# Kernel optimization log

Measured on AMD Instinct MI355X. Metric: run time of the kernel, lower is better.

The kernel has to match this reference:

```python
import jax, jax.numpy as jnp
import numpy as np

B, S, C = 8, 2048, 1024
DROPOUT_RATE = 0.1


def setup_inputs() -> dict:
    key = jax.random.key(0)
    k1, k2, k3 = jax.random.split(key, 3)
    x = jax.random.normal(k1, (B, S, C), dtype=jnp.float32)
    # Fixed orthogonal projection buffer, as in __init__: U from SVD of a random matrix
    rand_mat = jax.random.normal(k2, (C, C), dtype=jnp.float32)
    U, _, _ = jnp.linalg.svd(rand_mat)
    U = U.astype(jnp.float32)
    # Base random permutation of [0, C)
    perm = jax.random.permutation(k3, C).astype(jnp.int32)
    # Stand-in for random.randint(0, 1000), fixed for determinism
    randint = 123
    return {"x": x, "U": U, "perm": perm, "randint": randint}


def reference(x, U, perm, randint):
    # channel_dim == -1, so the transpose in the original forward is a no-op.
    rand_scale = (DROPOUT_RATE / (1.0 - DROPOUT_RATE)) ** 0.5
    n = x.shape[-1]
    b = x.size // n
    # _randperm_like: per-row permutation ans[b_, i] = perm[i] * (6*randint*b_ + 1) mod n.
    # Reduce the multiplier mod n first so int32 arithmetic never overflows
    # (math is identical since (a*b) % n == (a*(b%n)) % n).
    batch_rand = (jnp.arange(b, dtype=jnp.int32) * (randint * 6) + 1) % n  # [b]
    ans = (perm[None, :] * batch_rand[:, None]) % n                        # [b, n]
    ans = ans.reshape(x.shape)                                             # same shape as x

    x_g = jnp.take_along_axis(x, ans, axis=-1)   # gather per-row permuted channels
    y = jnp.matmul(x_g, U)                        # shared (C,C) projection
    # scatter_(-1, ans, y) places y[..., j] at position ans[..., j]; since ans is a
    # permutation per row, this equals gathering y with the inverse permutation.
    inv = jnp.argsort(ans, axis=-1)
    x_next = jnp.take_along_axis(y, inv, axis=-1)
    return x_next * rand_scale + x
```

## Files before the change

### kernel.cpp

```cpp
#include <hip/hip_runtime.h>
#include <hip/hip_bf16.h>

#define WS_UT    ((size_t)0)
#define WS_XG    ((size_t)2*1024*1024)

typedef __attribute__((ext_vector_type(8))) short short8;
typedef __attribute__((ext_vector_type(4))) float floatx4;

__device__ __forceinline__ void load_lds16(const void* g, void* l) {
  __builtin_amdgcn_global_load_lds(
      (const __attribute__((address_space(1))) void*)g,
      (__attribute__((address_space(3))) void*)l, 16, 0, 0);
}

__device__ __forceinline__ unsigned short f2bf(float f) {
  __hip_bfloat16 h = __float2bfloat16(f);
  return __builtin_bit_cast(unsigned short, h);
}
__device__ __forceinline__ float bf2f(unsigned short u) {
  return __uint_as_float(((unsigned)u) << 16);
}

__global__ void __launch_bounds__(256) prep_gather_k(const float* __restrict__ U,
                                                     const float* __restrict__ x,
                                                     const int* __restrict__ perm,
                                                     const int* __restrict__ prand,
                                                     unsigned short* __restrict__ ut,
                                                     unsigned short* __restrict__ xg) {
  __shared__ __align__(16) char smem[64 * 65 * 4];
  if (blockIdx.x < 256) {
    float (*tile)[65] = (float (*)[65])smem;
    const int tn = (blockIdx.x & 15) * 64;
    const int tk = (blockIdx.x >> 4) * 64;
    const int r = threadIdx.x >> 6;
    const int c = threadIdx.x & 63;
    for (int s = 0; s < 16; ++s)
      tile[s * 4 + r][c] = U[(size_t)(tk + s * 4 + r) * 1024 + tn + c];
    __syncthreads();
    for (int s = 0; s < 16; ++s)
      ut[(size_t)(tn + s * 4 + r) * 1024 + tk + c] = f2bf(tile[c][s * 4 + r]);
    return;
  }
  float (*xrow)[1024] = (float (*)[1024])smem;
  const int w = threadIdx.x >> 6, lane = threadIdx.x & 63;
  const int row = (blockIdx.x - 256) * 4 + w;
  const unsigned mult = ((unsigned)prand[0] * 6u) & 1023u;
  const unsigned br = (((unsigned)row & 1023u) * mult + 1u) & 1023u;
  const float* xr = x + (size_t)row * 1024;
  unsigned short* xo = xg + (size_t)row * 1024;
  for (int t = 0; t < 4; ++t) {
    floatx4 v = *(const floatx4*)(xr + t * 256 + lane * 4);
    *(floatx4*)(&xrow[w][t * 256 + lane * 4]) = v;
  }
  __syncthreads();
  for (int t = 0; t < 4; ++t) {
    int i0 = t * 256 + lane * 4;
    int4 p = *(const int4*)(perm + i0);
    ushort4 o;
    o.x = f2bf(xrow[w][((unsigned)p.x * br) & 1023u]);
    o.y = f2bf(xrow[w][((unsigned)p.y * br) & 1023u]);
    o.z = f2bf(xrow[w][((unsigned)p.z * br) & 1023u]);
    o.w = f2bf(xrow[w][((unsigned)p.w * br) & 1023u]);
    *(ushort4*)(xo + i0) = o;
  }
}

__global__ void __launch_bounds__(512, 2) gemm_scatter_k(
    const unsigned short* __restrict__ xg,
    const unsigned short* __restrict__ ut,
    const int* __restrict__ perm,
    const int* __restrict__ prand,
    float* __restrict__ out) {
  extern __shared__ __align__(16) char smem[];
  const int tid = threadIdx.x;
  const int w = tid >> 6, lane = tid & 63;
  const int m = lane & 15, q = lane >> 4;
  const int R0 = blockIdx.x * 64;
  const int wn = w * 128;

  const int swz0 = (q ^ (m & 7)) * 16;
  const int vA0 = m * 128 + swz0;
  const int vA1 = vA0 ^ 64;
  const int vB0 = 24576 + w * 16384 + m * 128 + swz0;
  const int vB1 = vB0 ^ 64;

  const unsigned short* asrc =
      xg + (size_t)(R0 + (tid >> 3)) * 1024 + (size_t)(((tid & 7) ^ ((tid >> 3) & 7)) * 8);
  const unsigned short* bsrc0 =
      ut + (size_t)(wn + (lane >> 3)) * 1024 + (size_t)(((lane & 7) ^ (lane >> 3)) * 8);
  char* bdst0 = smem + 24576 + w * 16384 + lane * 16;

  floatx4 acc[4][8];
#pragma unroll
  for (int i = 0; i < 4; ++i)
#pragma unroll
    for (int jj = 0; jj < 8; ++jj) acc[i][jj] = (floatx4)0.0f;

  load_lds16(asrc, smem + tid * 16);
#pragma unroll
  for (int t = 0; t < 16; ++t)
    load_lds16(bsrc0 + (size_t)t * 8192, bdst0 + t * 1024);
  load_lds16(asrc + 64, smem + 8192 + tid * 16);
  asm volatile("s_waitcnt vmcnt(1)" ::: "memory");
  __builtin_amdgcn_sched_barrier(0);
  __builtin_amdgcn_s_barrier();
  __builtin_amdgcn_sched_barrier(0);

#pragma unroll
  for (int kt = 0; kt < 16; ++kt) {
    const int ab = (kt % 3) * 8192;
    short8 a0[4];
#pragma unroll
    for (int i = 0; i < 4; ++i)
      a0[i] = *(const short8*)(smem + ab + i * 2048 + vA0);
    if (kt > 0) {
      asm volatile("s_waitcnt vmcnt(1)" ::: "memory");
      __builtin_amdgcn_sched_barrier(0);
    }
    __builtin_amdgcn_s_setprio(1);
#pragma unroll
    for (int jj = 0; jj < 8; ++jj) {
      short8 b = *(const short8*)(smem + jj * 2048 + vB0);
#pragma unroll
      for (int i = 0; i < 4; ++i)
        acc[i][jj] = __builtin_amdgcn_mfma_f32_16x16x32_bf16(b, a0[i], acc[i][jj], 0, 0, 0);
    }
    short8 a1[4];
#pragma unroll
    for (int i = 0; i < 4; ++i)
      a1[i] = *(const short8*)(smem + ab + i * 2048 + vA1);
#pragma unroll
    for (int jj = 0; jj < 8; ++jj) {
      short8 b = *(const short8*)(smem + jj * 2048 + vB1);
#pragma unroll
      for (int i = 0; i < 4; ++i)
        acc[i][jj] = __builtin_amdgcn_mfma_f32_16x16x32_bf16(b, a1[i], acc[i][jj], 0, 0, 0);
    }
    __builtin_amdgcn_s_setprio(0);
    if (kt < 15) {
      asm volatile("s_waitcnt lgkmcnt(0)" ::: "memory");
      __builtin_amdgcn_sched_barrier(0);
      const int k1 = (kt + 1) * 64;
#pragma unroll
      for (int t = 0; t < 16; ++t)
        load_lds16(bsrc0 + (size_t)t * 8192 + k1, bdst0 + t * 1024);
      if (kt < 14)
        load_lds16(asrc + (size_t)(kt + 2) * 64, smem + ((kt + 2) % 3) * 8192 + tid * 16);
      if (kt < 14) asm volatile("s_waitcnt vmcnt(17)" ::: "memory");
      else         asm volatile("s_waitcnt vmcnt(16)" ::: "memory");
      __builtin_amdgcn_sched_barrier(0);
      __builtin_amdgcn_s_barrier();
      __builtin_amdgcn_sched_barrier(0);
    }
  }
  __syncthreads();

  const unsigned mult = ((unsigned)prand[0] * 6u) & 1023u;
  const float rs = 0.33333334f;
  float* sbuf = (float*)(smem + 24576);
#pragma unroll
  for (int p = 0; p < 8; ++p) {
    const int i = p >> 1;
    if ((m >> 3) == (p & 1)) {
      const int r = i * 16 + m;
      const unsigned br = (((unsigned)(R0 + r) & 1023u) * mult + 1u) & 1023u;
      const unsigned short* xr = xg + (size_t)(R0 + r) * 1024;
#pragma unroll
      for (int jj = 0; jj < 8; ++jj) {
        const int j0 = wn + jj * 16 + q * 4;
        const int4 p4 = *(const int4*)(perm + j0);
        const ushort4 x4 = *(const ushort4*)(xr + j0);
        sbuf[((r & 7) << 10) + (((unsigned)p4.x * br) & 1023u)] = rs * acc[i][jj][0] + bf2f(x4.x);
        sbuf[((r & 7) << 10) + (((unsigned)p4.y * br) & 1023u)] = rs * acc[i][jj][1] + bf2f(x4.y);
        sbuf[((r & 7) << 10) + (((unsigned)p4.z * br) & 1023u)] = rs * acc[i][jj][2] + bf2f(x4.z);
        sbuf[((r & 7) << 10) + (((unsigned)p4.w * br) & 1023u)] = rs * acc[i][jj][3] + bf2f(x4.w);
      }
    }
    __syncthreads();
    float* orow = out + (size_t)(R0 + p * 8) * 1024;
#pragma unroll
    for (int v = 0; v < 4; ++v) {
      const int f = v * 512 + tid;
      *(floatx4*)(orow + (size_t)f * 4) = *(const floatx4*)(sbuf + (size_t)f * 4);
    }
    if (p < 7) __syncthreads();
  }
}

extern "C" void kernel_launch(void* const* d_in, const int* in_sizes, int n_in,
                              void* d_out, int out_size, void* d_ws, size_t ws_size,
                              hipStream_t stream) {
  const float* x = (const float*)d_in[0];
  const float* U = (const float*)d_in[1];
  const int* perm = (const int*)d_in[2];
  const int* prand = (const int*)d_in[3];
  float* out = (float*)d_out;
  char* ws = (char*)d_ws;
  unsigned short* ut = (unsigned short*)(ws + WS_UT);
  unsigned short* xg = (unsigned short*)(ws + WS_XG);

  hipFuncSetAttribute((const void*)gemm_scatter_k,
                      hipFuncAttributeMaxDynamicSharedMemorySize, 155648);

  prep_gather_k<<<256 + 4096, 256, 0, stream>>>(U, x, perm, prand, ut, xg);
  gemm_scatter_k<<<256, 512, 155648, stream>>>(xg, ut, perm, prand, out);
}
```

Baseline: 165.7 us.

## Double-buffer B in GEMM with K=32 steps and per-block rotated K start

Rewrites the GEMM main loop to use 32-wide K steps. B tiles are now double-buffered in LDS instead of single-buffered, which removes the wait on B reloads before each compute step, and A stays triple-buffered. Each block starts its K loop at a rotated offset (blockIdx & 31) so blocks spread their reads of the shared U matrix across different addresses instead of hitting the same tiles at once. The change adds more barriers per K element and a longer, more complex pipeline prologue and epilogue.

```diff
diff --git a/kernel.cpp b/kernel.cpp
--- a/kernel.cpp
+++ b/kernel.cpp
@@ -77,18 +77,18 @@
   const int m = lane & 15, q = lane >> 4;
   const int R0 = blockIdx.x * 64;
   const int wn = w * 128;
-
-  const int swz0 = (q ^ (m & 7)) * 16;
-  const int vA0 = m * 128 + swz0;
-  const int vA1 = vA0 ^ 64;
-  const int vB0 = 24576 + w * 16384 + m * 128 + swz0;
-  const int vB1 = vB0 ^ 64;
-
-  const unsigned short* asrc =
-      xg + (size_t)(R0 + (tid >> 3)) * 1024 + (size_t)(((tid & 7) ^ ((tid >> 3) & 7)) * 8);
-  const unsigned short* bsrc0 =
-      ut + (size_t)(wn + (lane >> 3)) * 1024 + (size_t)(((lane & 7) ^ (lane >> 3)) * 8);
-  char* bdst0 = smem + 24576 + w * 16384 + lane * 16;
+  const int rot = blockIdx.x & 31;
+
+  const int swz = (q ^ (m & 3)) * 16;
+  const int rdA = m * 64 + swz;
+  const int rdB = 12288 + w * 8192 + m * 64 + swz;
+
+  const int sr = lane >> 2;
+  const int schunk = ((lane & 3) ^ (sr & 3)) * 8;
+  const unsigned short* asrc = xg + (size_t)(R0 + w * 16 + sr) * 1024 + schunk;
+  const unsigned short* bsrc = ut + (size_t)(wn + sr) * 1024 + schunk;
+  char* adst = smem + w * 1024 + lane * 16;
+  char* bdst = smem + 12288 + w * 8192 + lane * 16;
 
   floatx4 acc[4][8];
 #pragma unroll
@@ -96,68 +96,76 @@
 #pragma unroll
     for (int jj = 0; jj < 8; ++jj) acc[i][jj] = (floatx4)0.0f;
 
-  load_lds16(asrc, smem + tid * 16);
-#pragma unroll
-  for (int t = 0; t < 16; ++t)
-    load_lds16(bsrc0 + (size_t)t * 8192, bdst0 + t * 1024);
-  load_lds16(asrc + 64, smem + 8192 + tid * 16);
-  asm volatile("s_waitcnt vmcnt(1)" ::: "memory");
+  auto stageB = [&](int buf, int kp) {
+#pragma unroll
+    for (int t = 0; t < 8; ++t)
+      load_lds16(bsrc + (size_t)t * 16384 + kp * 32, bdst + buf + t * 1024);
+  };
+  auto compute = [&](int aoff, int boff) {
+    short8 a[4], b[8];
+#pragma unroll
+    for (int i = 0; i < 4; ++i)
+      a[i] = *(const short8*)(smem + aoff + i * 1024 + rdA);
+#pragma unroll
+    for (int jj = 0; jj < 8; ++jj)
+      b[jj] = *(const short8*)(smem + boff + jj * 1024 + rdB);
+    __builtin_amdgcn_s_setprio(1);
+#pragma unroll
+    for (int i = 0; i < 4; ++i)
+#pragma unroll
+      for (int jj = 0; jj < 8; ++jj)
+        acc[i][jj] = __builtin_amdgcn_mfma_f32_16x16x32_bf16(b[jj], a[i],
+                                                             acc[i][jj], 0, 0, 0);
+    __builtin_amdgcn_s_setprio(0);
+    asm volatile("s_waitcnt lgkmcnt(0)" ::: "memory");
+    __builtin_amdgcn_sched_barrier(0);
+  };
+
+  int kpn = (rot + 1) & 31, kpn2 = (rot + 2) & 31;
+  if (w < 4) {
+    load_lds16(asrc + rot * 32, adst);
+    load_lds16(asrc + kpn * 32, adst + 4096);
+  }
+  stageB(0, rot);
+
+  int pc = 0, pn = 4096, pn2 = 8192;
+  int bb = 0;
+#pragma unroll 1
+  for (int h = 0; h < 30; ++h) {
+    stageB(bb ^ 65536, kpn);
+    if (w < 4) {
+      load_lds16(asrc + kpn2 * 32, adst + pn2);
+      asm volatile("s_waitcnt vmcnt(9)" ::: "memory");
+    } else {
+      asm volatile("s_waitcnt vmcnt(8)" ::: "memory");
+    }
+    __builtin_amdgcn_sched_barrier(0);
+    __builtin_amdgcn_s_barrier();
+    __builtin_amdgcn_sched_barrier(0);
+    compute(pc, bb);
+    int t = pc; pc = pn; pn = pn2; pn2 = t;
+    bb ^= 65536;
+    kpn = kpn2; kpn2 = (kpn2 + 1) & 31;
+  }
+  stageB(bb ^ 65536, kpn);
+  if (w < 4) asm volatile("s_waitcnt vmcnt(9)" ::: "memory");
+  else       asm volatile("s_waitcnt vmcnt(8)" ::: "memory");
   __builtin_amdgcn_sched_barrier(0);
   __builtin_amdgcn_s_barrier();
   __builtin_amdgcn_sched_barrier(0);
-
-#pragma unroll
-  for (int kt = 0; kt < 16; ++kt) {
-    const int ab = (kt % 3) * 8192;
-    short8 a0[4];
-#pragma unroll
-    for (int i = 0; i < 4; ++i)
-      a0[i] = *(const short8*)(smem + ab + i * 2048 + vA0);
-    if (kt > 0) {
-      asm volatile("s_waitcnt vmcnt(1)" ::: "memory");
-      __builtin_amdgcn_sched_barrier(0);
-    }
-    __builtin_amdgcn_s_setprio(1);
-#pragma unroll
-    for (int jj = 0; jj < 8; ++jj) {
-      short8 b = *(const short8*)(smem + jj * 2048 + vB0);
-#pragma unroll
-      for (int i = 0; i < 4; ++i)
-        acc[i][jj] = __builtin_amdgcn_mfma_f32_16x16x32_bf16(b, a0[i], acc[i][jj], 0, 0, 0);
-    }
-    short8 a1[4];
-#pragma unroll
-    for (int i = 0; i < 4; ++i)
-      a1[i] = *(const short8*)(smem + ab + i * 2048 + vA1);
-#pragma unroll
-    for (int jj = 0; jj < 8; ++jj) {
-      short8 b = *(const short8*)(smem + jj * 2048 + vB1);
-#pragma unroll
-      for (int i = 0; i < 4; ++i)
-        acc[i][jj] = __builtin_amdgcn_mfma_f32_16x16x32_bf16(b, a1[i], acc[i][jj], 0, 0, 0);
-    }
-    __builtin_amdgcn_s_setprio(0);
-    if (kt < 15) {
-      asm volatile("s_waitcnt lgkmcnt(0)" ::: "memory");
-      __builtin_amdgcn_sched_barrier(0);
-      const int k1 = (kt + 1) * 64;
-#pragma unroll
-      for (int t = 0; t < 16; ++t)
-        load_lds16(bsrc0 + (size_t)t * 8192 + k1, bdst0 + t * 1024);
-      if (kt < 14)
-        load_lds16(asrc + (size_t)(kt + 2) * 64, smem + ((kt + 2) % 3) * 8192 + tid * 16);
-      if (kt < 14) asm volatile("s_waitcnt vmcnt(17)" ::: "memory");
-      else         asm volatile("s_waitcnt vmcnt(16)" ::: "memory");
-      __builtin_amdgcn_sched_barrier(0);
-      __builtin_amdgcn_s_barrier();
-      __builtin_amdgcn_sched_barrier(0);
-    }
-  }
+  compute(pc, bb);
+  { int t = pc; pc = pn; pn = pn2; pn2 = t; }
+  bb ^= 65536;
+  asm volatile("s_waitcnt vmcnt(0)" ::: "memory");
+  __builtin_amdgcn_sched_barrier(0);
+  __builtin_amdgcn_s_barrier();
+  __builtin_amdgcn_sched_barrier(0);
+  compute(pc, bb);
   __syncthreads();
 
   const unsigned mult = ((unsigned)prand[0] * 6u) & 1023u;
   const float rs = 0.33333334f;
-  float* sbuf = (float*)(smem + 24576);
+  float* sbuf = (float*)smem;
 #pragma unroll
   for (int p = 0; p < 8; ++p) {
     const int i = p >> 1;
@@ -200,8 +208,8 @@
   unsigned short* xg = (unsigned short*)(ws + WS_XG);
 
   hipFuncSetAttribute((const void*)gemm_scatter_k,
-                      hipFuncAttributeMaxDynamicSharedMemorySize, 155648);
+                      hipFuncAttributeMaxDynamicSharedMemorySize, 143360);
 
   prep_gather_k<<<256 + 4096, 256, 0, stream>>>(U, x, perm, prand, ut, xg);
-  gemm_scatter_k<<<256, 512, 155648, stream>>>(xg, ut, perm, prand, out);
-}
+  gemm_scatter_k<<<256, 512, 143360, stream>>>(xg, ut, perm, prand, out);
+}
```

Result: slower. 174.0 us (+5.0%).

## Load GEMM A operand directly to registers and double-buffer B without barriers

Applied to the files above, without the earlier changes.

Replaces LDS staging of the gathered activation tile with direct per-wave global loads into registers, prefetched one K-step ahead. B tiles are double-buffered per wave in LDS with 32-wide K steps and a new swizzle, removing workgroup barriers from the main loop and cutting LDS allocation. The cost is redundant global/L2 reads of A by each of the eight waves and twice as many loop iterations.

```diff
diff --git a/kernel.cpp b/kernel.cpp
--- a/kernel.cpp
+++ b/kernel.cpp
@@ -78,17 +78,18 @@
   const int R0 = blockIdx.x * 64;
   const int wn = w * 128;
 
-  const int swz0 = (q ^ (m & 7)) * 16;
-  const int vA0 = m * 128 + swz0;
-  const int vA1 = vA0 ^ 64;
-  const int vB0 = 24576 + w * 16384 + m * 128 + swz0;
-  const int vB1 = vB0 ^ 64;
+  const int swz = (q ^ ((m >> 1) & 3)) * 16;
+  const int rdB = w * 16384 + m * 64 + swz;
 
-  const unsigned short* asrc =
-      xg + (size_t)(R0 + (tid >> 3)) * 1024 + (size_t)(((tid & 7) ^ ((tid >> 3) & 7)) * 8);
-  const unsigned short* bsrc0 =
-      ut + (size_t)(wn + (lane >> 3)) * 1024 + (size_t)(((lane & 7) ^ (lane >> 3)) * 8);
-  char* bdst0 = smem + 24576 + w * 16384 + lane * 16;
+  const int sr = lane >> 2;
+  const int schunk = ((lane & 3) ^ ((lane >> 3) & 3)) * 8;
+  const unsigned short* bsrc = ut + (size_t)(wn + sr) * 1024 + schunk;
+  char* bdst = smem + w * 16384 + lane * 16;
+
+  const unsigned short* ua[4];
+#pragma unroll
+  for (int i = 0; i < 4; ++i) ua[i] = xg + (size_t)(R0 + i * 16) * 1024;
+  const int va = m * 1024 + q * 8;
 
   floatx4 acc[4][8];
 #pragma unroll
@@ -96,68 +97,51 @@
 #pragma unroll
     for (int jj = 0; jj < 8; ++jj) acc[i][jj] = (floatx4)0.0f;
 
-  load_lds16(asrc, smem + tid * 16);
 #pragma unroll
-  for (int t = 0; t < 16; ++t)
-    load_lds16(bsrc0 + (size_t)t * 8192, bdst0 + t * 1024);
-  load_lds16(asrc + 64, smem + 8192 + tid * 16);
-  asm volatile("s_waitcnt vmcnt(1)" ::: "memory");
-  __builtin_amdgcn_sched_barrier(0);
-  __builtin_amdgcn_s_barrier();
-  __builtin_amdgcn_sched_barrier(0);
+  for (int t = 0; t < 8; ++t)
+    load_lds16(bsrc + (size_t)t * 16384, bdst + t * 1024);
+  short8 acur[4];
+#pragma unroll
+  for (int i = 0; i < 4; ++i) acur[i] = *(const short8*)(ua[i] + va);
 
 #pragma unroll
-  for (int kt = 0; kt < 16; ++kt) {
-    const int ab = (kt % 3) * 8192;
-    short8 a0[4];
+  for (int kt = 0; kt < 32; ++kt) {
+    const int buf = (kt & 1) * 8192;
+    short8 anxt[4];
+    if (kt < 31) {
+      const int k1 = (kt + 1) * 32;
+#pragma unroll
+      for (int t = 0; t < 8; ++t)
+        load_lds16(bsrc + (size_t)t * 16384 + k1, bdst + (buf ^ 8192) + t * 1024);
+#pragma unroll
+      for (int i = 0; i < 4; ++i) anxt[i] = *(const short8*)(ua[i] + va + k1);
+    }
+    __builtin_amdgcn_sched_barrier(0);
+    if (kt < 31) asm volatile("s_waitcnt vmcnt(16)" ::: "memory");
+    else         asm volatile("s_waitcnt vmcnt(0)" ::: "memory");
+    __builtin_amdgcn_sched_barrier(0);
+    short8 b[8];
+#pragma unroll
+    for (int jj = 0; jj < 8; ++jj)
+      b[jj] = *(const short8*)(smem + buf + jj * 1024 + rdB);
+    __builtin_amdgcn_s_setprio(1);
 #pragma unroll
     for (int i = 0; i < 4; ++i)
-      a0[i] = *(const short8*)(smem + ab + i * 2048 + vA0);
-    if (kt > 0) {
-      asm volatile("s_waitcnt vmcnt(1)" ::: "memory");
-      __builtin_amdgcn_sched_barrier(0);
-    }
-    __builtin_amdgcn_s_setprio(1);
 #pragma unroll
-    for (int jj = 0; jj < 8; ++jj) {
-      short8 b = *(const short8*)(smem + jj * 2048 + vB0);
+      for (int jj = 0; jj < 8; ++jj)
+        acc[i][jj] = __builtin_amdgcn_mfma_f32_16x16x32_bf16(b[jj], acur[i],
+                                                             acc[i][jj], 0, 0, 0);
+    __builtin_amdgcn_s_setprio(0);
+    asm volatile("s_waitcnt lgkmcnt(0)" ::: "memory");
+    __builtin_amdgcn_sched_barrier(0);
 #pragma unroll
-      for (int i = 0; i < 4; ++i)
-        acc[i][jj] = __builtin_amdgcn_mfma_f32_16x16x32_bf16(b, a0[i], acc[i][jj], 0, 0, 0);
-    }
-    short8 a1[4];
-#pragma unroll
-    for (int i = 0; i < 4; ++i)
-      a1[i] = *(const short8*)(smem + ab + i * 2048 + vA1);
-#pragma unroll
-    for (int jj = 0; jj < 8; ++jj) {
-      short8 b = *(const short8*)(smem + jj * 2048 + vB1);
-#pragma unroll
-      for (int i = 0; i < 4; ++i)
-        acc[i][jj] = __builtin_amdgcn_mfma_f32_16x16x32_bf16(b, a1[i], acc[i][jj], 0, 0, 0);
-    }
-    __builtin_amdgcn_s_setprio(0);
-    if (kt < 15) {
-      asm volatile("s_waitcnt lgkmcnt(0)" ::: "memory");
-      __builtin_amdgcn_sched_barrier(0);
-      const int k1 = (kt + 1) * 64;
-#pragma unroll
-      for (int t = 0; t < 16; ++t)
-        load_lds16(bsrc0 + (size_t)t * 8192 + k1, bdst0 + t * 1024);
-      if (kt < 14)
-        load_lds16(asrc + (size_t)(kt + 2) * 64, smem + ((kt + 2) % 3) * 8192 + tid * 16);
-      if (kt < 14) asm volatile("s_waitcnt vmcnt(17)" ::: "memory");
-      else         asm volatile("s_waitcnt vmcnt(16)" ::: "memory");
-      __builtin_amdgcn_sched_barrier(0);
-      __builtin_amdgcn_s_barrier();
-      __builtin_amdgcn_sched_barrier(0);
-    }
+    for (int i = 0; i < 4; ++i) acur[i] = anxt[i];
   }
   __syncthreads();
 
   const unsigned mult = ((unsigned)prand[0] * 6u) & 1023u;
   const float rs = 0.33333334f;
-  float* sbuf = (float*)(smem + 24576);
+  float* sbuf = (float*)smem;
 #pragma unroll
   for (int p = 0; p < 8; ++p) {
     const int i = p >> 1;
@@ -200,8 +184,8 @@
   unsigned short* xg = (unsigned short*)(ws + WS_XG);
 
   hipFuncSetAttribute((const void*)gemm_scatter_k,
-                      hipFuncAttributeMaxDynamicSharedMemorySize, 155648);
+                      hipFuncAttributeMaxDynamicSharedMemorySize, 131072);
 
   prep_gather_k<<<256 + 4096, 256, 0, stream>>>(U, x, perm, prand, ut, xg);
-  gemm_scatter_k<<<256, 512, 155648, stream>>>(xg, ut, perm, prand, out);
+  gemm_scatter_k<<<256, 512, 131072, stream>>>(xg, ut, perm, prand, out);
 }
```

Result: slower. 184.1 us (+11.1%).
